# Optimization experiments

Measured on AMD Instinct MI355X. Metric: run time of the kernel, lower is better.

## Reference

```python
import jax, jax.numpy as jnp
import numpy as np

B = 524288   # batch of agents
N = 64       # neighbors (other agents)
H = 32       # hidden (hardcoded in original via zeros(1,32) and sqrt(32))
V = 256      # vocab_size
SCALE = np.float32(np.sqrt(32.0))  # original divides by sqrt(32) regardless of hidden


def setup_inputs() -> dict:
    key = jax.random.key(0)
    ks = jax.random.split(key, 24)
    lin = lambda k, i, o: (jax.random.normal(k, (i, o), jnp.float32) * (1.0 / np.sqrt(i)))
    inp = {
        'symbol': jax.random.randint(ks[0], (B,), 0, V, jnp.int32),
        'other_hidden': jax.random.normal(ks[1], (N, H), jnp.float32),
        'prev_hidden': jax.random.normal(ks[2], (B, H), jnp.float32),
        'emb': jax.random.normal(ks[3], (V, H), jnp.float32),
        'mem_gate': jnp.zeros((H,), jnp.float32),
        'Wm': lin(ks[4], H, H), 'bm': jnp.zeros((H,), jnp.float32),
        'Wq': lin(ks[5], H, H), 'bq': jnp.zeros((H,), jnp.float32),
        'Wk': lin(ks[6], H, H), 'bk': jnp.zeros((H,), jnp.float32),
        'Wv': lin(ks[7], H, H), 'bv': jnp.zeros((H,), jnp.float32),
        'W1': lin(ks[8], H, H), 'b1': jnp.zeros((H,), jnp.float32),
        'W2': lin(ks[9], H, H), 'b2': jnp.zeros((H,), jnp.float32),
        'W3': lin(ks[10], H, H), 'b3': jnp.zeros((H,), jnp.float32),
        'W4': lin(ks[11], H, H), 'b4': jnp.zeros((H,), jnp.float32),
        'Wa': lin(ks[12], H, 1), 'ba': jnp.zeros((1,), jnp.float32),
        'Ws': lin(ks[13], H, V), 'bs': jnp.zeros((V,), jnp.float32),
        'Wi': lin(ks[14], H, 3), 'bi': jnp.zeros((3,), jnp.float32),
    }
    return inp


def reference(symbol, other_hidden, prev_hidden, emb, mem_gate,
              Wm, bm, Wq, bq, Wk, bk, Wv, bv,
              W1, b1, W2, b2, W3, b3, W4, b4,
              Wa, ba, Ws, bs, Wi, bi):
    # embedding lookup
    h = emb[symbol]                                   # [B, H]
    # gated memory update
    gate = jax.nn.sigmoid(mem_gate)                   # [H]
    mem = jnp.tanh(prev_hidden @ Wm + bm)             # [B, H]
    h = h * (1.0 - gate) + mem * gate
    # social attention over shared neighbor set
    q = h @ Wq + bq                                   # [B, H]
    k = other_hidden @ Wk + bk                        # [N, H]
    v = other_hidden @ Wv + bv                        # [N, H]
    scores = (q @ k.T) / SCALE                        # [B, N]
    weights = jax.nn.softmax(scores, axis=-1)
    h = h + (weights @ v) * 0.3
    for W, b in ((W1, b1), (W2, b2), (W3, b3), (W4, b4)):
        h = h + jnp.tanh(h @ W + b) * 0.3
    # output heads
    action = jnp.tanh(h @ Wa + ba)                    # [B, 1]
    symbol_pred = h @ Ws + bs                         # [B, V]
    intent = h @ Wi + bi                              # [B, 3]
    return (action, symbol_pred, intent, h)
```

## Files before the change

### kernel.cpp

```cpp
#include <hip/hip_runtime.h>
#include <hip/hip_bf16.h>

constexpr int BTOT = 524288;
constexpr int NN   = 64;
constexpr int H    = 32;
constexpr int V    = 256;

typedef __attribute__((ext_vector_type(4))) float f32x4;
typedef __attribute__((ext_vector_type(4))) int   int4v;
typedef __attribute__((ext_vector_type(8))) short short8;

union FragU { int4v i; short8 s; };

__device__ __forceinline__ float fast_rcp(float x){ return __builtin_amdgcn_rcpf(x); }
__device__ __forceinline__ float fast_tanh(float x){
    float e = __expf(2.0f * x);
    return 1.0f - 2.0f * fast_rcp(e + 1.0f);
}
__device__ __forceinline__ int pkbf(float lo, float hi){
    union { __hip_bfloat162 h2; int i; } u;
    u.h2.x = __float2bfloat16(lo);
    u.h2.y = __float2bfloat16(hi);
    return u.i;
}

__device__ int   g_Wfrag [6*2*64*4];
__device__ int   g_Kfrag [4*64*4];
__device__ int   g_Vfrag [2*2*64*4];
__device__ int   g_Wsfrag[16*64*4];
__device__ float g_biasd [6*64*8];
__device__ float g_gated [64*8];
__device__ float g_wad   [64*8];
__device__ float g_wid   [64*24];

__global__ void precompute(const float* __restrict__ other_hidden,
                           const float* __restrict__ mem_gate,
                           const float* __restrict__ Wk, const float* __restrict__ bk,
                           const float* __restrict__ Wv, const float* __restrict__ bv,
                           const float* __restrict__ Wm, const float* __restrict__ bm,
                           const float* __restrict__ Wq, const float* __restrict__ bq,
                           const float* __restrict__ W1, const float* __restrict__ b1,
                           const float* __restrict__ W2, const float* __restrict__ b2,
                           const float* __restrict__ W3, const float* __restrict__ b3,
                           const float* __restrict__ W4, const float* __restrict__ b4,
                           const float* __restrict__ Wa, const float* __restrict__ Wi,
                           const float* __restrict__ Ws)
{
    __shared__ float Kst[64][32];
    __shared__ float Vst[64][32];
    __shared__ float gateS[32];
    const int t = threadIdx.x;

    if (t < 32) gateS[t] = fast_rcp(1.0f + __expf(-mem_gate[t]));
    {
        int n = t >> 2, c = (t & 3) * 8;
        float ak[8], av[8];
        #pragma unroll
        for (int i = 0; i < 8; ++i){ ak[i] = bk[c+i]; av[i] = bv[c+i]; }
        #pragma unroll
        for (int j = 0; j < H; ++j){
            float x = other_hidden[n*H + j];
            #pragma unroll
            for (int i = 0; i < 8; ++i){
                ak[i] = fmaf(x, Wk[j*H + c + i], ak[i]);
                av[i] = fmaf(x, Wv[j*H + c + i], av[i]);
            }
        }
        #pragma unroll
        for (int i = 0; i < 8; ++i){ Kst[n][c+i] = ak[i]; Vst[n][c+i] = av[i]; }
    }
    __syncthreads();

    #pragma unroll
    for (int w = 0; w < 6; ++w){
        const float* W = (w==0)?Wm : (w==1)?Wq : (w==2)?W1 : (w==3)?W2 : (w==4)?W3 : W4;
        for (int e = t; e < 128; e += 256){
            int mt = e >> 6, l = e & 63, la = l & 15, g = l >> 4;
            int m = mt*16 + la;
            int base = ((w*2 + mt)*64 + l)*4;
            #pragma unroll
            for (int j = 0; j < 4; ++j){
                int k0 = g*8 + 2*j;
                g_Wfrag[base + j] = pkbf(W[k0*H + m], W[(k0+1)*H + m]);
            }
        }
    }
    #pragma unroll
    for (int w = 0; w < 6; ++w){
        const float* bp_ = (w==0)?bm : (w==1)?bq : (w==2)?b1 : (w==3)?b2 : (w==4)?b3 : b4;
        for (int e = t; e < 512; e += 256){
            int l = e >> 3, idx = e & 7, mt = idx >> 2, r = idx & 3;
            int F = mt*16 + ((l>>4)&3)*4 + r;
            g_biasd[(w*64 + l)*8 + idx] = bp_[F];
        }
    }
    {
        int e = t;
        int mt = e >> 6, l = e & 63, la = l & 15, g = l >> 4;
        int n = mt*16 + la;
        #pragma unroll
        for (int j = 0; j < 4; ++j){
            int k0 = g*8 + 2*j;
            g_Kfrag[e*4 + j] = pkbf(Kst[n][k0], Kst[n][k0+1]);
        }
    }
    {
        int e = t;
        int mt = e >> 7, kt = (e >> 6) & 1, l = e & 63, la = l & 15, g = l >> 4;
        int m = mt*16 + la;
        #pragma unroll
        for (int j = 0; j < 4; ++j){
            int n0 = kt*32 + g*8 + 2*j;
            g_Vfrag[e*4 + j] = pkbf(Vst[n0][m], Vst[n0+1][m]);
        }
    }
    for (int e = t; e < 1024; e += 256){
        int mt = e >> 6, l = e & 63, la = l & 15, g = l >> 4;
        int m = mt*16 + la;
        #pragma unroll
        for (int j = 0; j < 4; ++j){
            int k0 = g*8 + 2*j;
            g_Wsfrag[e*4 + j] = pkbf(Ws[k0*V + m], Ws[(k0+1)*V + m]);
        }
    }
    for (int e = t; e < 512; e += 256){
        int l = e >> 3, idx = e & 7;
        int F = (idx>>2)*16 + ((l>>4)&3)*4 + (idx&3);
        g_gated[e] = gateS[F];
        g_wad[e]   = Wa[F];
    }
    for (int e = t; e < 1536; e += 256){
        int l = e / 24, m2 = e % 24, fidx = m2 / 3, j = m2 % 3;
        int F = (fidx>>2)*16 + ((l>>4)&3)*4 + (fidx&3);
        g_wid[e] = Wi[F*3 + j];
    }
}

__device__ __forceinline__ FragU d2b(f32x4 m0, f32x4 m1, int idxA, int idxB, bool glo){
    int p0a = pkbf(m0[0], m0[1]);
    int p1a = pkbf(m0[2], m0[3]);
    int p0b = pkbf(m1[0], m1[1]);
    int p1b = pkbf(m1[2], m1[3]);
    int tA0  = __builtin_amdgcn_ds_bpermute(idxA, p0a);
    int tA0b = __builtin_amdgcn_ds_bpermute(idxA, p0b);
    int tA1  = __builtin_amdgcn_ds_bpermute(idxA, p1a);
    int tA1b = __builtin_amdgcn_ds_bpermute(idxA, p1b);
    int tB0  = __builtin_amdgcn_ds_bpermute(idxB, p0a);
    int tB0b = __builtin_amdgcn_ds_bpermute(idxB, p0b);
    int tB1  = __builtin_amdgcn_ds_bpermute(idxB, p1a);
    int tB1b = __builtin_amdgcn_ds_bpermute(idxB, p1b);
    FragU r;
    r.i = int4v{ glo ? tA0 : tA0b, glo ? tA1 : tA1b,
                 glo ? tB0 : tB0b, glo ? tB1 : tB1b };
    return r;
}

__device__ __forceinline__ float bred_sum(float v, int bx16, int bx32){
    v += __int_as_float(__builtin_amdgcn_ds_bpermute(bx16, __float_as_int(v)));
    v += __int_as_float(__builtin_amdgcn_ds_bpermute(bx32, __float_as_int(v)));
    return v;
}
__device__ __forceinline__ float bred_max(float v, int bx16, int bx32){
    v = fmaxf(v, __int_as_float(__builtin_amdgcn_ds_bpermute(bx16, __float_as_int(v))));
    v = fmaxf(v, __int_as_float(__builtin_amdgcn_ds_bpermute(bx32, __float_as_int(v))));
    return v;
}
__device__ __forceinline__ f32x4 tanh4(f32x4 v){
    f32x4 r;
    r[0] = fast_tanh(v[0]); r[1] = fast_tanh(v[1]);
    r[2] = fast_tanh(v[2]); r[3] = fast_tanh(v[3]);
    return r;
}

#define MFMA(a, b, c) __builtin_amdgcn_mfma_f32_16x16x32_bf16((a), (b), (c), 0, 0, 0)

__global__ __launch_bounds__(256, 2) void social_main(
    const int*   __restrict__ symbol,
    const float* __restrict__ prev_hidden,
    const float* __restrict__ emb,
    const float* __restrict__ bs,
    const float* __restrict__ ba,
    const float* __restrict__ bi,
    float* __restrict__ out)
{
    const int tid = threadIdx.x;
    const int wv = tid >> 6, l = tid & 63;
    const int la = l & 15, g = l >> 4;
    const bool glo = (g < 2);
    const int idxA = (((g & 1) << 5) + la) << 2;
    const int idxB = idxA + 64;
    const int bx16 = (l ^ 16) << 2;
    const int bx32 = (l ^ 32) << 2;
    const int A0 = blockIdx.x * 128 + wv * 32;

    __shared__ float ldsAll[4][1088];
    __shared__ float bsS[256];
    float* lbase = ldsAll[wv];

    bsS[tid] = bs[tid];
    __syncthreads();

    float* out_action = out;
    float* out_sym    = out + (size_t)BTOT;
    float* out_int    = out + (size_t)BTOT * (1 + V);
    float* out_h      = out + (size_t)BTOT * (1 + V + 3);

    const int4v* WF = reinterpret_cast<const int4v*>(g_Wfrag);
    const int4v* KF = reinterpret_cast<const int4v*>(g_Kfrag);
    const int4v* VF = reinterpret_cast<const int4v*>(g_Vfrag);
    const int4v* SF = reinterpret_cast<const int4v*>(g_Wsfrag);
    const f32x4 zero4 = {0.f, 0.f, 0.f, 0.f};

    FragU phb[2];
    #pragma unroll
    for (int nt = 0; nt < 2; ++nt){
        const f32x4* p = reinterpret_cast<const f32x4*>(
            prev_hidden + (size_t)(A0 + nt*16 + la) * H + g*8);
        f32x4 v0 = p[0], v1 = p[1];
        phb[nt].i = int4v{ pkbf(v0[0],v0[1]), pkbf(v0[2],v0[3]),
                           pkbf(v1[0],v1[1]), pkbf(v1[2],v1[3]) };
    }

    f32x4 h_[2][2];
    {
        f32x4 bias[2];
        bias[0] = *reinterpret_cast<const f32x4*>(g_biasd + l*8);
        bias[1] = *reinterpret_cast<const f32x4*>(g_biasd + l*8 + 4);
        f32x4 m_[2][2];
        #pragma unroll
        for (int mt = 0; mt < 2; ++mt){
            FragU af; af.i = WF[(0*2 + mt)*64 + l];
            #pragma unroll
            for (int nt = 0; nt < 2; ++nt)
                m_[mt][nt] = MFMA(af.s, phb[nt].s, bias[mt]);
        }
        f32x4 gt[2];
        gt[0] = *reinterpret_cast<const f32x4*>(g_gated + l*8);
        gt[1] = *reinterpret_cast<const f32x4*>(g_gated + l*8 + 4);
        int sym0 = symbol[A0 + la], sym1 = symbol[A0 + 16 + la];
        #pragma unroll
        for (int mt = 0; mt < 2; ++mt)
        #pragma unroll
        for (int nt = 0; nt < 2; ++nt){
            const float* eb = emb + (size_t)(nt ? sym1 : sym0)*H + mt*16 + g*4;
            #pragma unroll
            for (int r = 0; r < 4; ++r){
                float gv = gt[mt][r];
                h_[mt][nt][r] = eb[r]*(1.0f - gv) + fast_tanh(m_[mt][nt][r])*gv;
            }
        }
    }

    f32x4 q_[2][2];
    {
        f32x4 bias[2];
        bias[0] = *reinterpret_cast<const f32x4*>(g_biasd + 512 + l*8);
        bias[1] = *reinterpret_cast<const f32x4*>(g_biasd + 512 + l*8 + 4);
        FragU hb[2] = { d2b(h_[0][0], h_[1][0], idxA, idxB, glo),
                        d2b(h_[0][1], h_[1][1], idxA, idxB, glo) };
        #pragma unroll
        for (int mt = 0; mt < 2; ++mt){
            FragU af; af.i = WF[(1*2 + mt)*64 + l];
            #pragma unroll
            for (int nt = 0; nt < 2; ++nt)
                q_[mt][nt] = MFMA(af.s, hb[nt].s, bias[mt]);
        }
    }

    f32x4 s_[4][2];
    {
        FragU qb[2] = { d2b(q_[0][0], q_[1][0], idxA, idxB, glo),
                        d2b(q_[0][1], q_[1][1], idxA, idxB, glo) };
        #pragma unroll
        for (int mt = 0; mt < 4; ++mt){
            FragU af; af.i = KF[mt*64 + l];
            #pragma unroll
            for (int nt = 0; nt < 2; ++nt)
                s_[mt][nt] = MFMA(af.s, qb[nt].s, zero4);
        }
    }

    const float INVS = 0.17677669529663687f;
    float coef[2];
    #pragma unroll
    for (int nt = 0; nt < 2; ++nt){
        float mx = s_[0][nt][0];
        #pragma unroll
        for (int mt = 0; mt < 4; ++mt)
        #pragma unroll
        for (int r = 0; r < 4; ++r) mx = fmaxf(mx, s_[mt][nt][r]);
        mx = bred_max(mx, bx16, bx32);
        float den = 0.f;
        #pragma unroll
        for (int mt = 0; mt < 4; ++mt)
        #pragma unroll
        for (int r = 0; r < 4; ++r){
            float w = __expf((s_[mt][nt][r] - mx) * INVS);
            s_[mt][nt][r] = w;
            den += w;
        }
        den = bred_sum(den, bx16, bx32);
        coef[nt] = 0.3f * fast_rcp(den);
    }

    {
        FragU wb[2][2];
        #pragma unroll
        for (int kt = 0; kt < 2; ++kt)
        #pragma unroll
        for (int nt = 0; nt < 2; ++nt)
            wb[kt][nt] = d2b(s_[2*kt][nt], s_[2*kt+1][nt], idxA, idxB, glo);
        #pragma unroll
        for (int mt = 0; mt < 2; ++mt){
            FragU vf0, vf1;
            vf0.i = VF[(mt*2 + 0)*64 + l];
            vf1.i = VF[(mt*2 + 1)*64 + l];
            #pragma unroll
            for (int nt = 0; nt < 2; ++nt){
                f32x4 acc = MFMA(vf0.s, wb[0][nt].s, zero4);
                acc = MFMA(vf1.s, wb[1][nt].s, acc);
                h_[mt][nt] += acc * coef[nt];
            }
        }
    }

    for (int blk = 0; blk < 4; ++blk){
        f32x4 bias[2];
        bias[0] = *reinterpret_cast<const f32x4*>(g_biasd + (2+blk)*512 + l*8);
        bias[1] = *reinterpret_cast<const f32x4*>(g_biasd + (2+blk)*512 + l*8 + 4);
        FragU hb[2] = { d2b(h_[0][0], h_[1][0], idxA, idxB, glo),
                        d2b(h_[0][1], h_[1][1], idxA, idxB, glo) };
        #pragma unroll
        for (int mt = 0; mt < 2; ++mt){
            FragU af; af.i = WF[((2+blk)*2 + mt)*64 + l];
            #pragma unroll
            for (int nt = 0; nt < 2; ++nt){
                f32x4 tv = MFMA(af.s, hb[nt].s, bias[mt]);
                h_[mt][nt] += 0.3f * tanh4(tv);
            }
        }
    }

    FragU hb[2] = { d2b(h_[0][0], h_[1][0], idxA, idxB, glo),
                    d2b(h_[0][1], h_[1][1], idxA, idxB, glo) };
    FragU sf[16];
    #pragma unroll
    for (int mt = 0; mt < 16; ++mt)
        sf[mt].i = SF[mt*64 + l];

    {
        union { f32x4 v[2]; float s[8]; } wa;
        wa.v[0] = *reinterpret_cast<const f32x4*>(g_wad + l*8);
        wa.v[1] = *reinterpret_cast<const f32x4*>(g_wad + l*8 + 4);
        float ba0 = ba[0];
        float act[2];
        #pragma unroll
        for (int nt = 0; nt < 2; ++nt){
            float acc = 0.f;
            #pragma unroll
            for (int mt = 0; mt < 2; ++mt)
            #pragma unroll
            for (int r = 0; r < 4; ++r)
                acc = fmaf(h_[mt][nt][r], wa.s[mt*4 + r], acc);
            acc = bred_sum(acc, bx16, bx32);
            act[nt] = fast_tanh(acc + ba0);
        }
        if (l < 16){
            out_action[A0 + la]      = act[0];
            out_action[A0 + 16 + la] = act[1];
        }
    }

    {
        union { f32x4 v[6]; float s[24]; } wi;
        #pragma unroll
        for (int k = 0; k < 6; ++k)
            wi.v[k] = *(reinterpret_cast<const f32x4*>(g_wid + l*24) + k);
        float bi0 = bi[0], bi1 = bi[1], bi2 = bi[2];
        #pragma unroll
        for (int nt = 0; nt < 2; ++nt){
            float i0 = 0.f, i1 = 0.f, i2 = 0.f;
            #pragma unroll
            for (int mt = 0; mt < 2; ++mt)
            #pragma unroll
            for (int r = 0; r < 4; ++r){
                float hv = h_[mt][nt][r];
                int base = (mt*4 + r)*3;
                i0 = fmaf(hv, wi.s[base + 0], i0);
                i1 = fmaf(hv, wi.s[base + 1], i1);
                i2 = fmaf(hv, wi.s[base + 2], i2);
            }
            i0 = bred_sum(i0, bx16, bx32) + bi0;
            i1 = bred_sum(i1, bx16, bx32) + bi1;
            i2 = bred_sum(i2, bx16, bx32) + bi2;
            if (l < 16){
                size_t a = (size_t)(A0 + nt*16 + la);
                out_int[a*3 + 0] = i0;
                out_int[a*3 + 1] = i1;
                out_int[a*3 + 2] = i2;
            }
        }
    }

    {
        float* buf = lbase;
        #pragma unroll
        for (int mt = 0; mt < 2; ++mt)
        #pragma unroll
        for (int nt = 0; nt < 2; ++nt){
            int wb0 = (nt*16 + la)*33 + mt*16 + g*4;
            buf[wb0 + 0] = h_[mt][nt][0];
            buf[wb0 + 1] = h_[mt][nt][1];
            buf[wb0 + 2] = h_[mt][nt][2];
            buf[wb0 + 3] = h_[mt][nt][3];
        }
        int c = l & 7;
        #pragma unroll
        for (int j = 0; j < 4; ++j){
            int ag = j*8 + (l >> 3);
            f32x4 ov;
            ov[0] = buf[ag*33 + c*4 + 0];
            ov[1] = buf[ag*33 + c*4 + 1];
            ov[2] = buf[ag*33 + c*4 + 2];
            ov[3] = buf[ag*33 + c*4 + 3];
            *reinterpret_cast<f32x4*>(out_h + (size_t)(A0 + ag)*H + c*4) = ov;
        }
    }

    {
        int c2 = l & 3, rr = l >> 2;
        #pragma unroll
        for (int mt = 0; mt < 16; ++mt){
            f32x4 o0 = MFMA(sf[mt].s, hb[0].s, zero4);
            f32x4 o1 = MFMA(sf[mt].s, hb[1].s, zero4);
            float* buf = lbase + (mt & 1)*544;
            int w0 = la*17 + g*4;
            int w1 = (16 + la)*17 + g*4;
            buf[w0+0] = o0[0]; buf[w0+1] = o0[1]; buf[w0+2] = o0[2]; buf[w0+3] = o0[3];
            buf[w1+0] = o1[0]; buf[w1+1] = o1[1]; buf[w1+2] = o1[2]; buf[w1+3] = o1[3];
            f32x4 bv = *reinterpret_cast<const f32x4*>(bsS + mt*16 + c2*4);
            #pragma unroll
            for (int j = 0; j < 2; ++j){
                int ag = j*16 + rr;
                f32x4 ov;
                ov[0] = buf[ag*17 + c2*4 + 0] + bv[0];
                ov[1] = buf[ag*17 + c2*4 + 1] + bv[1];
                ov[2] = buf[ag*17 + c2*4 + 2] + bv[2];
                ov[3] = buf[ag*17 + c2*4 + 3] + bv[3];
                *reinterpret_cast<f32x4*>(out_sym + (size_t)(A0 + ag)*V + mt*16 + c2*4) = ov;
            }
        }
    }
}

extern "C" void kernel_launch(void* const* d_in, const int* in_sizes, int n_in,
                              void* d_out, int out_size, void* d_ws, size_t ws_size,
                              hipStream_t stream)
{
    const int*   symbol       = (const int*)  d_in[0];
    const float* other_hidden = (const float*)d_in[1];
    const float* prev_hidden  = (const float*)d_in[2];
    const float* emb          = (const float*)d_in[3];
    const float* mem_gate     = (const float*)d_in[4];
    const float* Wm  = (const float*)d_in[5];  const float* bm = (const float*)d_in[6];
    const float* Wq  = (const float*)d_in[7];  const float* bq = (const float*)d_in[8];
    const float* Wk  = (const float*)d_in[9];  const float* bk = (const float*)d_in[10];
    const float* Wv  = (const float*)d_in[11]; const float* bv = (const float*)d_in[12];
    const float* W1  = (const float*)d_in[13]; const float* b1 = (const float*)d_in[14];
    const float* W2  = (const float*)d_in[15]; const float* b2 = (const float*)d_in[16];
    const float* W3  = (const float*)d_in[17]; const float* b3 = (const float*)d_in[18];
    const float* W4  = (const float*)d_in[19]; const float* b4 = (const float*)d_in[20];
    const float* Wa  = (const float*)d_in[21]; const float* ba = (const float*)d_in[22];
    const float* Wsm = (const float*)d_in[23]; const float* bs = (const float*)d_in[24];
    const float* Wi  = (const float*)d_in[25]; const float* bi = (const float*)d_in[26];

    precompute<<<1, 256, 0, stream>>>(other_hidden, mem_gate, Wk, bk, Wv, bv,
                                      Wm, bm, Wq, bq, W1, b1, W2, b2, W3, b3, W4, b4,
                                      Wa, Wi, Wsm);

    social_main<<<BTOT / 128, 256, 0, stream>>>(symbol, prev_hidden, emb, bs, ba, bi,
                                                (float*)d_out);
}
```

Measured before the change: 164.1 us.

## Process four tiles per block with LDS-staged weights and prefetched inputs

Each block now handles four 128-agent tiles in a loop instead of one. The precomputed weight fragments, biases, gate and head weights are staged once into LDS and reused across the tiles. The next tile's prev_hidden, symbols and embedding rows are prefetched into registers while the current tile computes. This amortizes the per-block weight loads and overlaps global-load latency with MFMA work, at the cost of more registers and LDS per block, which may reduce occupancy, and a four-times smaller grid.

```diff
diff --git a/kernel.cpp b/kernel.cpp
--- a/kernel.cpp
+++ b/kernel.cpp
@@ -5,6 +5,7 @@
 constexpr int NN   = 64;
 constexpr int H    = 32;
 constexpr int V    = 256;
+constexpr int TPB  = 4;
 
 typedef __attribute__((ext_vector_type(4))) float f32x4;
 typedef __attribute__((ext_vector_type(4))) int   int4v;
@@ -24,14 +25,14 @@
     return u.i;
 }
 
-__device__ int   g_Wfrag [6*2*64*4];
-__device__ int   g_Kfrag [4*64*4];
-__device__ int   g_Vfrag [2*2*64*4];
-__device__ int   g_Wsfrag[16*64*4];
-__device__ float g_biasd [6*64*8];
-__device__ float g_gated [64*8];
-__device__ float g_wad   [64*8];
-__device__ float g_wid   [64*24];
+__device__ __attribute__((aligned(16))) int   g_Wfrag [6*2*64*4];
+__device__ __attribute__((aligned(16))) int   g_Kfrag [4*64*4];
+__device__ __attribute__((aligned(16))) int   g_Vfrag [2*2*64*4];
+__device__ __attribute__((aligned(16))) int   g_Wsfrag[16*64*4];
+__device__ __attribute__((aligned(16))) float g_biasd [6*64*8];
+__device__ __attribute__((aligned(16))) float g_gated [64*8];
+__device__ __attribute__((aligned(16))) float g_wad   [64*8];
+__device__ __attribute__((aligned(16))) float g_wid   [64*24];
 
 __global__ void precompute(const float* __restrict__ other_hidden,
                            const float* __restrict__ mem_gate,
@@ -191,13 +192,34 @@
     const int idxB = idxA + 64;
     const int bx16 = (l ^ 16) << 2;
     const int bx32 = (l ^ 32) << 2;
-    const int A0 = blockIdx.x * 128 + wv * 32;
-
+
+    __shared__ int4v sWF[768];
+    __shared__ int4v sKF[256];
+    __shared__ int4v sVF[256];
+    __shared__ f32x4 sBiasd[768];
+    __shared__ f32x4 sGated[128];
+    __shared__ f32x4 sWad[128];
+    __shared__ float sWid[1536];
+    __shared__ float sBs[256];
     __shared__ float ldsAll[4][1088];
-    __shared__ float bsS[256];
     float* lbase = ldsAll[wv];
 
-    bsS[tid] = bs[tid];
+    {
+        const int4v* q4 = reinterpret_cast<const int4v*>(g_Wfrag);
+        for (int i = tid; i < 768; i += 256) sWF[i] = q4[i];
+        sKF[tid] = reinterpret_cast<const int4v*>(g_Kfrag)[tid];
+        sVF[tid] = reinterpret_cast<const int4v*>(g_Vfrag)[tid];
+        const f32x4* qf = reinterpret_cast<const f32x4*>(g_biasd);
+        for (int i = tid; i < 768; i += 256) sBiasd[i] = qf[i];
+        if (tid < 128){
+            sGated[tid] = reinterpret_cast<const f32x4*>(g_gated)[tid];
+            sWad[tid]   = reinterpret_cast<const f32x4*>(g_wad)[tid];
+        }
+        const f32x4* qw = reinterpret_cast<const f32x4*>(g_wid);
+        for (int i = tid; i < 384; i += 256)
+            reinterpret_cast<f32x4*>(sWid)[i] = qw[i];
+        sBs[tid] = bs[tid];
+    }
     __syncthreads();
 
     float* out_action = out;
@@ -205,249 +227,294 @@
     float* out_int    = out + (size_t)BTOT * (1 + V);
     float* out_h      = out + (size_t)BTOT * (1 + V + 3);
 
-    const int4v* WF = reinterpret_cast<const int4v*>(g_Wfrag);
-    const int4v* KF = reinterpret_cast<const int4v*>(g_Kfrag);
-    const int4v* VF = reinterpret_cast<const int4v*>(g_Vfrag);
     const int4v* SF = reinterpret_cast<const int4v*>(g_Wsfrag);
     const f32x4 zero4 = {0.f, 0.f, 0.f, 0.f};
 
-    FragU phb[2];
+    const int base = blockIdx.x * (128*TPB) + wv*32;
+
+    const float ba0 = ba[0];
+    const float bi0 = bi[0], bi1 = bi[1], bi2 = bi[2];
+
+    f32x4 pv[2][2][2];
+    f32x4 em[2][2][2];
+    int syn0[2], syn1[2];
+
+    {
+        #pragma unroll
+        for (int nt = 0; nt < 2; ++nt){
+            const f32x4* p = reinterpret_cast<const f32x4*>(
+                prev_hidden + (size_t)(base + nt*16 + la)*H + g*8);
+            pv[0][nt][0] = p[0]; pv[0][nt][1] = p[1];
+        }
+        int s0 = symbol[base + la], s1 = symbol[base + 16 + la];
+        syn0[1] = symbol[base + 128 + la];
+        syn1[1] = symbol[base + 128 + 16 + la];
+        #pragma unroll
+        for (int mt = 0; mt < 2; ++mt)
+        #pragma unroll
+        for (int nt = 0; nt < 2; ++nt)
+            em[0][mt][nt] = *reinterpret_cast<const f32x4*>(
+                emb + (size_t)(nt ? s1 : s0)*H + mt*16 + g*4);
+    }
+
     #pragma unroll
-    for (int nt = 0; nt < 2; ++nt){
-        const f32x4* p = reinterpret_cast<const f32x4*>(
-            prev_hidden + (size_t)(A0 + nt*16 + la) * H + g*8);
-        f32x4 v0 = p[0], v1 = p[1];
-        phb[nt].i = int4v{ pkbf(v0[0],v0[1]), pkbf(v0[2],v0[3]),
-                           pkbf(v1[0],v1[1]), pkbf(v1[2],v1[3]) };
-    }
-
-    f32x4 h_[2][2];
-    {
-        f32x4 bias[2];
-        bias[0] = *reinterpret_cast<const f32x4*>(g_biasd + l*8);
-        bias[1] = *reinterpret_cast<const f32x4*>(g_biasd + l*8 + 4);
-        f32x4 m_[2][2];
-        #pragma unroll
-        for (int mt = 0; mt < 2; ++mt){
-            FragU af; af.i = WF[(0*2 + mt)*64 + l];
+    for (int t = 0; t < TPB; ++t){
+        const int c  = t & 1;
+        const int nx = c ^ 1;
+        const int A0 = base + t*128;
+
+        FragU phb[2];
+        #pragma unroll
+        for (int nt = 0; nt < 2; ++nt)
+            phb[nt].i = int4v{ pkbf(pv[c][nt][0][0], pv[c][nt][0][1]),
+                               pkbf(pv[c][nt][0][2], pv[c][nt][0][3]),
+                               pkbf(pv[c][nt][1][0], pv[c][nt][1][1]),
+                               pkbf(pv[c][nt][1][2], pv[c][nt][1][3]) };
+
+        if (t + 1 < TPB){
+            const int A1 = base + (t+1)*128;
+            #pragma unroll
+            for (int nt = 0; nt < 2; ++nt){
+                const f32x4* p = reinterpret_cast<const f32x4*>(
+                    prev_hidden + (size_t)(A1 + nt*16 + la)*H + g*8);
+                pv[nx][nt][0] = p[0]; pv[nx][nt][1] = p[1];
+            }
+        }
+        if (t + 2 < TPB){
+            const int A2 = base + (t+2)*128;
+            syn0[c] = symbol[A2 + la];
+            syn1[c] = symbol[A2 + 16 + la];
+        }
+
+        f32x4 h_[2][2];
+        {
+            f32x4 bias0 = sBiasd[l*2], bias1 = sBiasd[l*2 + 1];
+            f32x4 m_[2][2];
+            #pragma unroll
+            for (int mt = 0; mt < 2; ++mt){
+                FragU af; af.i = sWF[(0*2 + mt)*64 + l];
+                #pragma unroll
+                for (int nt = 0; nt < 2; ++nt)
+                    m_[mt][nt] = MFMA(af.s, phb[nt].s, mt ? bias1 : bias0);
+            }
+            f32x4 gt0 = sGated[l*2], gt1 = sGated[l*2 + 1];
+            #pragma unroll
+            for (int mt = 0; mt < 2; ++mt)
+            #pragma unroll
+            for (int nt = 0; nt < 2; ++nt){
+                #pragma unroll
+                for (int r = 0; r < 4; ++r){
+                    float gv = mt ? gt1[r] : gt0[r];
+                    h_[mt][nt][r] = em[c][mt][nt][r]*(1.0f - gv)
+                                  + fast_tanh(m_[mt][nt][r])*gv;
+                }
+            }
+        }
+
+        if (t + 1 < TPB){
+            int a0 = syn0[nx], a1 = syn1[nx];
+            #pragma unroll
+            for (int mt = 0; mt < 2; ++mt)
             #pragma unroll
             for (int nt = 0; nt < 2; ++nt)
-                m_[mt][nt] = MFMA(af.s, phb[nt].s, bias[mt]);
-        }
-        f32x4 gt[2];
-        gt[0] = *reinterpret_cast<const f32x4*>(g_gated + l*8);
-        gt[1] = *reinterpret_cast<const f32x4*>(g_gated + l*8 + 4);
-        int sym0 = symbol[A0 + la], sym1 = symbol[A0 + 16 + la];
-        #pragma unroll
-        for (int mt = 0; mt < 2; ++mt)
+                em[nx][mt][nt] = *reinterpret_cast<const f32x4*>(
+                    emb + (size_t)(nt ? a1 : a0)*H + mt*16 + g*4);
+        }
+
+        f32x4 q_[2][2];
+        {
+            f32x4 bias0 = sBiasd[128 + l*2], bias1 = sBiasd[128 + l*2 + 1];
+            FragU hb0[2] = { d2b(h_[0][0], h_[1][0], idxA, idxB, glo),
+                             d2b(h_[0][1], h_[1][1], idxA, idxB, glo) };
+            #pragma unroll
+            for (int mt = 0; mt < 2; ++mt){
+                FragU af; af.i = sWF[(1*2 + mt)*64 + l];
+                #pragma unroll
+                for (int nt = 0; nt < 2; ++nt)
+                    q_[mt][nt] = MFMA(af.s, hb0[nt].s, mt ? bias1 : bias0);
+            }
+        }
+
+        f32x4 s_[4][2];
+        {
+            FragU qb[2] = { d2b(q_[0][0], q_[1][0], idxA, idxB, glo),
+                            d2b(q_[0][1], q_[1][1], idxA, idxB, glo) };
+            #pragma unroll
+            for (int mt = 0; mt < 4; ++mt){
+                FragU af; af.i = sKF[mt*64 + l];
+                #pragma unroll
+                for (int nt = 0; nt < 2; ++nt)
+                    s_[mt][nt] = MFMA(af.s, qb[nt].s, zero4);
+            }
+        }
+
+        const float INVS = 0.17677669529663687f;
+        float coef[2];
         #pragma unroll
         for (int nt = 0; nt < 2; ++nt){
-            const float* eb = emb + (size_t)(nt ? sym1 : sym0)*H + mt*16 + g*4;
+            float mx = s_[0][nt][0];
+            #pragma unroll
+            for (int mt = 0; mt < 4; ++mt)
+            #pragma unroll
+            for (int r = 0; r < 4; ++r) mx = fmaxf(mx, s_[mt][nt][r]);
+            mx = bred_max(mx, bx16, bx32);
+            float den = 0.f;
+            #pragma unroll
+            for (int mt = 0; mt < 4; ++mt)
             #pragma unroll
             for (int r = 0; r < 4; ++r){
-                float gv = gt[mt][r];
-                h_[mt][nt][r] = eb[r]*(1.0f - gv) + fast_tanh(m_[mt][nt][r])*gv;
-            }
-        }
-    }
-
-    f32x4 q_[2][2];
-    {
-        f32x4 bias[2];
-        bias[0] = *reinterpret_cast<const f32x4*>(g_biasd + 512 + l*8);
-        bias[1] = *reinterpret_cast<const f32x4*>(g_biasd + 512 + l*8 + 4);
+                float w = __expf((s_[mt][nt][r] - mx) * INVS);
+                s_[mt][nt][r] = w;
+                den += w;
+            }
+            den = bred_sum(den, bx16, bx32);
+            coef[nt] = 0.3f * fast_rcp(den);
+        }
+
+        {
+            FragU wb[2][2];
+            #pragma unroll
+            for (int kt = 0; kt < 2; ++kt)
+            #pragma unroll
+            for (int nt = 0; nt < 2; ++nt)
+                wb[kt][nt] = d2b(s_[2*kt][nt], s_[2*kt+1][nt], idxA, idxB, glo);
+            #pragma unroll
+            for (int mt = 0; mt < 2; ++mt){
+                FragU vf0, vf1;
+                vf0.i = sVF[(mt*2 + 0)*64 + l];
+                vf1.i = sVF[(mt*2 + 1)*64 + l];
+                #pragma unroll
+                for (int nt = 0; nt < 2; ++nt){
+                    f32x4 acc = MFMA(vf0.s, wb[0][nt].s, zero4);
+                    acc = MFMA(vf1.s, wb[1][nt].s, acc);
+                    h_[mt][nt] += acc * coef[nt];
+                }
+            }
+        }
+
+        #pragma unroll
+        for (int blk = 0; blk < 4; ++blk){
+            f32x4 bias0 = sBiasd[(2+blk)*128 + l*2];
+            f32x4 bias1 = sBiasd[(2+blk)*128 + l*2 + 1];
+            FragU hb1[2] = { d2b(h_[0][0], h_[1][0], idxA, idxB, glo),
+                             d2b(h_[0][1], h_[1][1], idxA, idxB, glo) };
+            #pragma unroll
+            for (int mt = 0; mt < 2; ++mt){
+                FragU af; af.i = sWF[((2+blk)*2 + mt)*64 + l];
+                #pragma unroll
+                for (int nt = 0; nt < 2; ++nt){
+                    f32x4 tv = MFMA(af.s, hb1[nt].s, mt ? bias1 : bias0);
+                    h_[mt][nt] += 0.3f * tanh4(tv);
+                }
+            }
+        }
+
         FragU hb[2] = { d2b(h_[0][0], h_[1][0], idxA, idxB, glo),
                         d2b(h_[0][1], h_[1][1], idxA, idxB, glo) };
-        #pragma unroll
-        for (int mt = 0; mt < 2; ++mt){
-            FragU af; af.i = WF[(1*2 + mt)*64 + l];
-            #pragma unroll
-            for (int nt = 0; nt < 2; ++nt)
-                q_[mt][nt] = MFMA(af.s, hb[nt].s, bias[mt]);
-        }
-    }
-
-    f32x4 s_[4][2];
-    {
-        FragU qb[2] = { d2b(q_[0][0], q_[1][0], idxA, idxB, glo),
-                        d2b(q_[0][1], q_[1][1], idxA, idxB, glo) };
-        #pragma unroll
-        for (int mt = 0; mt < 4; ++mt){
-            FragU af; af.i = KF[mt*64 + l];
-            #pragma unroll
-            for (int nt = 0; nt < 2; ++nt)
-                s_[mt][nt] = MFMA(af.s, qb[nt].s, zero4);
-        }
-    }
-
-    const float INVS = 0.17677669529663687f;
-    float coef[2];
-    #pragma unroll
-    for (int nt = 0; nt < 2; ++nt){
-        float mx = s_[0][nt][0];
-        #pragma unroll
-        for (int mt = 0; mt < 4; ++mt)
-        #pragma unroll
-        for (int r = 0; r < 4; ++r) mx = fmaxf(mx, s_[mt][nt][r]);
-        mx = bred_max(mx, bx16, bx32);
-        float den = 0.f;
-        #pragma unroll
-        for (int mt = 0; mt < 4; ++mt)
-        #pragma unroll
-        for (int r = 0; r < 4; ++r){
-            float w = __expf((s_[mt][nt][r] - mx) * INVS);
-            s_[mt][nt][r] = w;
-            den += w;
-        }
-        den = bred_sum(den, bx16, bx32);
-        coef[nt] = 0.3f * fast_rcp(den);
-    }
-
-    {
-        FragU wb[2][2];
-        #pragma unroll
-        for (int kt = 0; kt < 2; ++kt)
-        #pragma unroll
-        for (int nt = 0; nt < 2; ++nt)
-            wb[kt][nt] = d2b(s_[2*kt][nt], s_[2*kt+1][nt], idxA, idxB, glo);
-        #pragma unroll
-        for (int mt = 0; mt < 2; ++mt){
-            FragU vf0, vf1;
-            vf0.i = VF[(mt*2 + 0)*64 + l];
-            vf1.i = VF[(mt*2 + 1)*64 + l];
+        FragU sf[16];
+        #pragma unroll
+        for (int mt = 0; mt < 16; ++mt)
+            sf[mt].i = SF[mt*64 + l];
+
+        {
+            union { f32x4 v[2]; float s[8]; } wa;
+            wa.v[0] = sWad[l*2];
+            wa.v[1] = sWad[l*2 + 1];
+            float act[2];
             #pragma unroll
             for (int nt = 0; nt < 2; ++nt){
-                f32x4 acc = MFMA(vf0.s, wb[0][nt].s, zero4);
-                acc = MFMA(vf1.s, wb[1][nt].s, acc);
-                h_[mt][nt] += acc * coef[nt];
-            }
-        }
-    }
-
-    for (int blk = 0; blk < 4; ++blk){
-        f32x4 bias[2];
-        bias[0] = *reinterpret_cast<const f32x4*>(g_biasd + (2+blk)*512 + l*8);
-        bias[1] = *reinterpret_cast<const f32x4*>(g_biasd + (2+blk)*512 + l*8 + 4);
-        FragU hb[2] = { d2b(h_[0][0], h_[1][0], idxA, idxB, glo),
-                        d2b(h_[0][1], h_[1][1], idxA, idxB, glo) };
-        #pragma unroll
-        for (int mt = 0; mt < 2; ++mt){
-            FragU af; af.i = WF[((2+blk)*2 + mt)*64 + l];
+                float acc = 0.f;
+                #pragma unroll
+                for (int mt = 0; mt < 2; ++mt)
+                #pragma unroll
+                for (int r = 0; r < 4; ++r)
+                    acc = fmaf(h_[mt][nt][r], wa.s[mt*4 + r], acc);
+                acc = bred_sum(acc, bx16, bx32);
+                act[nt] = fast_tanh(acc + ba0);
+            }
+            if (l < 16){
+                out_action[A0 + la]      = act[0];
+                out_action[A0 + 16 + la] = act[1];
+            }
+        }
+
+        {
+            union { f32x4 v[6]; float s[24]; } wi;
+            const f32x4* wip = reinterpret_cast<const f32x4*>(sWid + l*24);
+            #pragma unroll
+            for (int k = 0; k < 6; ++k) wi.v[k] = wip[k];
             #pragma unroll
             for (int nt = 0; nt < 2; ++nt){
-                f32x4 tv = MFMA(af.s, hb[nt].s, bias[mt]);
-                h_[mt][nt] += 0.3f * tanh4(tv);
-            }
-        }
-    }
-
-    FragU hb[2] = { d2b(h_[0][0], h_[1][0], idxA, idxB, glo),
-                    d2b(h_[0][1], h_[1][1], idxA, idxB, glo) };
-    FragU sf[16];
-    #pragma unroll
-    for (int mt = 0; mt < 16; ++mt)
-        sf[mt].i = SF[mt*64 + l];
-
-    {
-        union { f32x4 v[2]; float s[8]; } wa;
-        wa.v[0] = *reinterpret_cast<const f32x4*>(g_wad + l*8);
-        wa.v[1] = *reinterpret_cast<const f32x4*>(g_wad + l*8 + 4);
-        float ba0 = ba[0];
-        float act[2];
-        #pragma unroll
-        for (int nt = 0; nt < 2; ++nt){
-            float acc = 0.f;
+                float i0 = 0.f, i1 = 0.f, i2 = 0.f;
+                #pragma unroll
+                for (int mt = 0; mt < 2; ++mt)
+                #pragma unroll
+                for (int r = 0; r < 4; ++r){
+                    float hv = h_[mt][nt][r];
+                    int bidx = (mt*4 + r)*3;
+                    i0 = fmaf(hv, wi.s[bidx + 0], i0);
+                    i1 = fmaf(hv, wi.s[bidx + 1], i1);
+                    i2 = fmaf(hv, wi.s[bidx + 2], i2);
+                }
+                i0 = bred_sum(i0, bx16, bx32) + bi0;
+                i1 = bred_sum(i1, bx16, bx32) + bi1;
+                i2 = bred_sum(i2, bx16, bx32) + bi2;
+                if (l < 16){
+                    size_t a = (size_t)(A0 + nt*16 + la);
+                    out_int[a*3 + 0] = i0;
+                    out_int[a*3 + 1] = i1;
+                    out_int[a*3 + 2] = i2;
+                }
+            }
+        }
+
+        {
+            float* buf = lbase;
             #pragma unroll
             for (int mt = 0; mt < 2; ++mt)
             #pragma unroll
-            for (int r = 0; r < 4; ++r)
-                acc = fmaf(h_[mt][nt][r], wa.s[mt*4 + r], acc);
-            acc = bred_sum(acc, bx16, bx32);
-            act[nt] = fast_tanh(acc + ba0);
-        }
-        if (l < 16){
-            out_action[A0 + la]      = act[0];
-            out_action[A0 + 16 + la] = act[1];
-        }
-    }
-
-    {
-        union { f32x4 v[6]; float s[24]; } wi;
-        #pragma unroll
-        for (int k = 0; k < 6; ++k)
-            wi.v[k] = *(reinterpret_cast<const f32x4*>(g_wid + l*24) + k);
-        float bi0 = bi[0], bi1 = bi[1], bi2 = bi[2];
-        #pragma unroll
-        for (int nt = 0; nt < 2; ++nt){
-            float i0 = 0.f, i1 = 0.f, i2 = 0.f;
-            #pragma unroll
-            for (int mt = 0; mt < 2; ++mt)
-            #pragma unroll
-            for (int r = 0; r < 4; ++r){
-                float hv = h_[mt][nt][r];
-                int base = (mt*4 + r)*3;
-                i0 = fmaf(hv, wi.s[base + 0], i0);
-                i1 = fmaf(hv, wi.s[base + 1], i1);
-                i2 = fmaf(hv, wi.s[base + 2], i2);
-            }
-            i0 = bred_sum(i0, bx16, bx32) + bi0;
-            i1 = bred_sum(i1, bx16, bx32) + bi1;
-            i2 = bred_sum(i2, bx16, bx32) + bi2;
-            if (l < 16){
-                size_t a = (size_t)(A0 + nt*16 + la);
-                out_int[a*3 + 0] = i0;
-                out_int[a*3 + 1] = i1;
-                out_int[a*3 + 2] = i2;
-            }
-        }
-    }
-
-    {
-        float* buf = lbase;
-        #pragma unroll
-        for (int mt = 0; mt < 2; ++mt)
-        #pragma unroll
-        for (int nt = 0; nt < 2; ++nt){
-            int wb0 = (nt*16 + la)*33 + mt*16 + g*4;
-            buf[wb0 + 0] = h_[mt][nt][0];
-            buf[wb0 + 1] = h_[mt][nt][1];
-            buf[wb0 + 2] = h_[mt][nt][2];
-            buf[wb0 + 3] = h_[mt][nt][3];
-        }
-        int c = l & 7;
-        #pragma unroll
-        for (int j = 0; j < 4; ++j){
-            int ag = j*8 + (l >> 3);
-            f32x4 ov;
-            ov[0] = buf[ag*33 + c*4 + 0];
-            ov[1] = buf[ag*33 + c*4 + 1];
-            ov[2] = buf[ag*33 + c*4 + 2];
-            ov[3] = buf[ag*33 + c*4 + 3];
-            *reinterpret_cast<f32x4*>(out_h + (size_t)(A0 + ag)*H + c*4) = ov;
-        }
-    }
-
-    {
-        int c2 = l & 3, rr = l >> 2;
-        #pragma unroll
-        for (int mt = 0; mt < 16; ++mt){
-            f32x4 o0 = MFMA(sf[mt].s, hb[0].s, zero4);
-            f32x4 o1 = MFMA(sf[mt].s, hb[1].s, zero4);
-            float* buf = lbase + (mt & 1)*544;
-            int w0 = la*17 + g*4;
-            int w1 = (16 + la)*17 + g*4;
-            buf[w0+0] = o0[0]; buf[w0+1] = o0[1]; buf[w0+2] = o0[2]; buf[w0+3] = o0[3];
-            buf[w1+0] = o1[0]; buf[w1+1] = o1[1]; buf[w1+2] = o1[2]; buf[w1+3] = o1[3];
-            f32x4 bv = *reinterpret_cast<const f32x4*>(bsS + mt*16 + c2*4);
-            #pragma unroll
-            for (int j = 0; j < 2; ++j){
-                int ag = j*16 + rr;
+            for (int nt = 0; nt < 2; ++nt){
+                int wb0 = (nt*16 + la)*33 + mt*16 + g*4;
+                buf[wb0 + 0] = h_[mt][nt][0];
+                buf[wb0 + 1] = h_[mt][nt][1];
+                buf[wb0 + 2] = h_[mt][nt][2];
+                buf[wb0 + 3] = h_[mt][nt][3];
+            }
+            int cc = l & 7;
+            #pragma unroll
+            for (int j = 0; j < 4; ++j){
+                int ag = j*8 + (l >> 3);
                 f32x4 ov;
-                ov[0] = buf[ag*17 + c2*4 + 0] + bv[0];
-                ov[1] = buf[ag*17 + c2*4 + 1] + bv[1];
-                ov[2] = buf[ag*17 + c2*4 + 2] + bv[2];
-                ov[3] = buf[ag*17 + c2*4 + 3] + bv[3];
-                *reinterpret_cast<f32x4*>(out_sym + (size_t)(A0 + ag)*V + mt*16 + c2*4) = ov;
+                ov[0] = buf[ag*33 + cc*4 + 0];
+                ov[1] = buf[ag*33 + cc*4 + 1];
+                ov[2] = buf[ag*33 + cc*4 + 2];
+                ov[3] = buf[ag*33 + cc*4 + 3];
+                *reinterpret_cast<f32x4*>(out_h + (size_t)(A0 + ag)*H + cc*4) = ov;
+            }
+        }
+
+        {
+            int c2 = l & 3, rr = l >> 2;
+            #pragma unroll
+            for (int mt = 0; mt < 16; ++mt){
+                f32x4 o0 = MFMA(sf[mt].s, hb[0].s, zero4);
+                f32x4 o1 = MFMA(sf[mt].s, hb[1].s, zero4);
+                float* buf = lbase + (mt & 1)*544;
+                int w0 = la*17 + g*4;
+                int w1 = (16 + la)*17 + g*4;
+                buf[w0+0] = o0[0]; buf[w0+1] = o0[1]; buf[w0+2] = o0[2]; buf[w0+3] = o0[3];
+                buf[w1+0] = o1[0]; buf[w1+1] = o1[1]; buf[w1+2] = o1[2]; buf[w1+3] = o1[3];
+                f32x4 bv = *reinterpret_cast<const f32x4*>(sBs + mt*16 + c2*4);
+                #pragma unroll
+                for (int j = 0; j < 2; ++j){
+                    int ag = j*16 + rr;
+                    f32x4 ov;
+                    ov[0] = buf[ag*17 + c2*4 + 0] + bv[0];
+                    ov[1] = buf[ag*17 + c2*4 + 1] + bv[1];
+                    ov[2] = buf[ag*17 + c2*4 + 2] + bv[2];
+                    ov[3] = buf[ag*17 + c2*4 + 3] + bv[3];
+                    *reinterpret_cast<f32x4*>(out_sym + (size_t)(A0 + ag)*V + mt*16 + c2*4) = ov;
+                }
             }
         }
     }
@@ -478,6 +545,6 @@
                                       Wm, bm, Wq, bq, W1, b1, W2, b2, W3, b3, W4, b4,
                                       Wa, Wi, Wsm);
 
-    social_main<<<BTOT / 128, 256, 0, stream>>>(symbol, prev_hidden, emb, bs, ba, bi,
-                                                (float*)d_out);
-}
+    social_main<<<BTOT / (128*TPB), 256, 0, stream>>>(symbol, prev_hidden, emb,
+                                                      bs, ba, bi, (float*)d_out);
+}
```

Result: slower. 183.8 us (+12.0%).

## Stage Ws fragments in shared memory and raise occupancy target to three blocks

Applied to the files above, without the earlier changes.

The 16 Ws MFMA fragments, previously preloaded into 64 VGPRs per lane, are now copied once per block into a 16 KB LDS array and read one at a time inside the symbol-prediction loop. The launch bound moves from 2 to 3 blocks per CU, so the register savings go toward more resident waves to hide the memory latency of this store-bound kernel. Each block now pays for a 16 KB global-to-LDS copy plus LDS reads in the output loop, and LDS per block grows to about 34 KB. Device arrays also get 16-byte alignment.

```diff
diff --git a/kernel.cpp b/kernel.cpp
--- a/kernel.cpp
+++ b/kernel.cpp
@@ -24,14 +24,14 @@
     return u.i;
 }
 
-__device__ int   g_Wfrag [6*2*64*4];
-__device__ int   g_Kfrag [4*64*4];
-__device__ int   g_Vfrag [2*2*64*4];
-__device__ int   g_Wsfrag[16*64*4];
-__device__ float g_biasd [6*64*8];
-__device__ float g_gated [64*8];
-__device__ float g_wad   [64*8];
-__device__ float g_wid   [64*24];
+__device__ __attribute__((aligned(16))) int   g_Wfrag [6*2*64*4];
+__device__ __attribute__((aligned(16))) int   g_Kfrag [4*64*4];
+__device__ __attribute__((aligned(16))) int   g_Vfrag [2*2*64*4];
+__device__ __attribute__((aligned(16))) int   g_Wsfrag[16*64*4];
+__device__ __attribute__((aligned(16))) float g_biasd [6*64*8];
+__device__ __attribute__((aligned(16))) float g_gated [64*8];
+__device__ __attribute__((aligned(16))) float g_wad   [64*8];
+__device__ __attribute__((aligned(16))) float g_wid   [64*24];
 
 __global__ void precompute(const float* __restrict__ other_hidden,
                            const float* __restrict__ mem_gate,
@@ -174,7 +174,7 @@
 
 #define MFMA(a, b, c) __builtin_amdgcn_mfma_f32_16x16x32_bf16((a), (b), (c), 0, 0, 0)
 
-__global__ __launch_bounds__(256, 2) void social_main(
+__global__ __launch_bounds__(256, 3) void social_main(
     const int*   __restrict__ symbol,
     const float* __restrict__ prev_hidden,
     const float* __restrict__ emb,
@@ -194,10 +194,15 @@
     const int A0 = blockIdx.x * 128 + wv * 32;
 
     __shared__ float ldsAll[4][1088];
+    __shared__ int4v sSF[1024];
     __shared__ float bsS[256];
     float* lbase = ldsAll[wv];
 
-    bsS[tid] = bs[tid];
+    {
+        const int4v* q4 = reinterpret_cast<const int4v*>(g_Wsfrag);
+        for (int i = tid; i < 1024; i += 256) sSF[i] = q4[i];
+        bsS[tid] = bs[tid];
+    }
     __syncthreads();
 
     float* out_action = out;
@@ -208,7 +213,6 @@
     const int4v* WF = reinterpret_cast<const int4v*>(g_Wfrag);
     const int4v* KF = reinterpret_cast<const int4v*>(g_Kfrag);
     const int4v* VF = reinterpret_cast<const int4v*>(g_Vfrag);
-    const int4v* SF = reinterpret_cast<const int4v*>(g_Wsfrag);
     const f32x4 zero4 = {0.f, 0.f, 0.f, 0.f};
 
     FragU phb[2];
@@ -343,10 +347,6 @@
 
     FragU hb[2] = { d2b(h_[0][0], h_[1][0], idxA, idxB, glo),
                     d2b(h_[0][1], h_[1][1], idxA, idxB, glo) };
-    FragU sf[16];
-    #pragma unroll
-    for (int mt = 0; mt < 16; ++mt)
-        sf[mt].i = SF[mt*64 + l];
 
     {
         union { f32x4 v[2]; float s[8]; } wa;
@@ -431,8 +431,9 @@
         int c2 = l & 3, rr = l >> 2;
         #pragma unroll
         for (int mt = 0; mt < 16; ++mt){
-            f32x4 o0 = MFMA(sf[mt].s, hb[0].s, zero4);
-            f32x4 o1 = MFMA(sf[mt].s, hb[1].s, zero4);
+            FragU af; af.i = sSF[mt*64 + l];
+            f32x4 o0 = MFMA(af.s, hb[0].s, zero4);
+            f32x4 o1 = MFMA(af.s, hb[1].s, zero4);
             float* buf = lbase + (mt & 1)*544;
             int w0 = la*17 + g*4;
             int w1 = (16 + la)*17 + g*4;
```

New measurement: 162.7 us. Within noise of the previous version (-0.9%).
